# Performance work log

Hardware: AMD Instinct MI355X
Metric: run time of the kernel (lower is better)

Reference implementation:

```python
import jax, jax.numpy as jnp
import numpy as np

N_QUBITS = 4


def _apply_rx(state, theta, wire):
    # state: [B, 2,2,2,2] complex64, theta: [B] real angles; RX on `wire`.
    st = jnp.moveaxis(state, wire + 1, -1)
    bshape = (theta.shape[0],) + (1,) * (st.ndim - 2)
    c = jnp.cos(theta * 0.5).reshape(bshape).astype(jnp.complex64)
    s = (-1j) * jnp.sin(theta * 0.5).reshape(bshape).astype(jnp.complex64)
    new = jnp.stack([c * st[..., 0] + s * st[..., 1],
                     s * st[..., 0] + c * st[..., 1]], axis=-1)
    return jnp.moveaxis(new, -1, wire + 1)


def _apply_cnot(state, control, target):
    st = jnp.moveaxis(state, (control + 1, target + 1), (-2, -1))
    new = jnp.stack([st[..., 0, :], st[..., 1, ::-1]], axis=-2)
    return jnp.moveaxis(new, (-2, -1), (control + 1, target + 1))


def _quantum_gate(angles, thetas):
    # angles: [B, n] data-encoding RX angles; thetas: [n] trainable RX angles.
    B, n = angles.shape
    state = jnp.zeros((B,) + (2,) * n, jnp.complex64)
    state = state.at[(slice(None),) + (0,) * n].set(1.0)  # |0...0>
    for w in range(n):
        state = _apply_rx(state, angles[:, w], w)
    for w in range(n):
        state = _apply_rx(state, jnp.broadcast_to(thetas[w], (B,)), w)
    for w in range(n):
        state = _apply_cnot(state, w, (w + 1) % n)
    probs = jnp.abs(state.reshape(B, 2 ** n)) ** 2  # [B, 16]
    bits = (np.arange(2 ** n)[:, None] >> np.arange(n - 1, -1, -1)[None, :]) & 1
    signs = jnp.asarray(1.0 - 2.0 * bits, jnp.float32)  # [16, n] PauliZ eigvals
    return probs @ signs  # [B, n] <Z_w> expectations


def setup_inputs() -> dict:
    key = jax.random.key(0)
    ks = jax.random.split(key, 12)
    B, D, H, n = 131072, 256, 4, N_QUBITS
    fan_in = D + H
    sc = 1.0 / np.sqrt(fan_in)
    inp = {
        'x': jax.random.normal(ks[0], (B, D), jnp.float32),
        'hx': jax.random.normal(ks[1], (B, H), jnp.float32),
        'cx': jax.random.normal(ks[2], (B, H), jnp.float32),
        'W_f': jax.random.normal(ks[3], (n, fan_in), jnp.float32) * sc,
        'b_f': jnp.zeros((n,), jnp.float32),
        'W_i': jax.random.normal(ks[4], (n, fan_in), jnp.float32) * sc,
        'b_i': jnp.zeros((n,), jnp.float32),
        'W_u': jax.random.normal(ks[5], (n, fan_in), jnp.float32) * sc,
        'b_u': jnp.zeros((n,), jnp.float32),
        'W_o': jax.random.normal(ks[6], (n, fan_in), jnp.float32) * sc,
        'b_o': jnp.zeros((n,), jnp.float32),
        'th_f': jax.random.normal(ks[7], (n,), jnp.float32),
        'th_i': jax.random.normal(ks[8], (n,), jnp.float32),
        'th_u': jax.random.normal(ks[9], (n,), jnp.float32),
        'th_o': jax.random.normal(ks[10], (n,), jnp.float32),
    }
    return inp


def reference(x, hx, cx, W_f, b_f, W_i, b_i, W_u, b_u, W_o, b_o,
              th_f, th_i, th_u, th_o):
    comb = jnp.concatenate([x, hx], axis=1)  # [B, D+H]
    f = jax.nn.sigmoid(_quantum_gate(comb @ W_f.T + b_f, th_f))
    i = jax.nn.sigmoid(_quantum_gate(comb @ W_i.T + b_i, th_i))
    g = jnp.tanh(_quantum_gate(comb @ W_u.T + b_u, th_u))
    o = jax.nn.sigmoid(_quantum_gate(comb @ W_o.T + b_o, th_o))
    c_new = f * cx + i * g
    h_new = o * jnp.tanh(c_new)
    return (h_new, c_new)
```

## Files before the change

kernel.cpp:

```cpp
#include <hip/hip_runtime.h>

#define NB   131072
#define TPB  256
#define FANIN 260

__device__ __forceinline__ float sigm_(float x) { return 1.0f / (1.0f + __expf(-x)); }
__device__ __forceinline__ float tanh_(float x) { return 1.0f - 2.0f / (__expf(2.0f * x) + 1.0f); }

__global__ void qlstm_prep(const float* __restrict__ Wf, const float* __restrict__ bf,
                           const float* __restrict__ Wi, const float* __restrict__ bi,
                           const float* __restrict__ Wu, const float* __restrict__ bu,
                           const float* __restrict__ Wo, const float* __restrict__ bo,
                           const float* __restrict__ thf, const float* __restrict__ thi,
                           const float* __restrict__ thu, const float* __restrict__ tho,
                           float* __restrict__ Wp, float* __restrict__ bth) {
    int t = blockIdx.x * blockDim.x + threadIdx.x;
    if (t < FANIN * 16) {
        int k = t >> 4, gw = t & 15, g = gw >> 2, w = gw & 3;
        const float* Wg = (g == 0) ? Wf : (g == 1) ? Wi : (g == 2) ? Wu : Wo;
        Wp[t] = Wg[w * FANIN + k];
    }
    if (t < 16) {
        int g = t >> 2, w = t & 3;
        const float* bg = (g == 0) ? bf  : (g == 1) ? bi  : (g == 2) ? bu  : bo;
        const float* tg = (g == 0) ? thf : (g == 1) ? thi : (g == 2) ? thu : tho;
        bth[t] = bg[w] + tg[w];
    }
}

__global__ __launch_bounds__(TPB) void qlstm_main(
        const float* __restrict__ x, const float* __restrict__ hx,
        const float* __restrict__ cx, const float* __restrict__ Wp,
        const float* __restrict__ bth, float* __restrict__ out) {
    __shared__ float xs[TPB * 33];

    const int tid  = threadIdx.x;
    const int row0 = blockIdx.x * TPB;
    const int row  = row0 + tid;

    float acc[16];
#pragma unroll
    for (int j = 0; j < 16; ++j) acc[j] = 0.0f;

    const float4* x4 = (const float4*)x;

    for (int stage = 0; stage < 8; ++stage) {
#pragma unroll
        for (int u = 0; u < 8; ++u) {
            int f  = tid + (u << 8);
            int r  = f >> 3;
            int c4 = f & 7;
            float4 v = x4[(size_t)(row0 + r) * 64 + stage * 8 + c4];
            float* dst = &xs[r * 33 + (c4 << 2)];
            dst[0] = v.x; dst[1] = v.y; dst[2] = v.z; dst[3] = v.w;
        }
        __syncthreads();

        const float* xrow = &xs[tid * 33];
        const float* wbase = Wp + stage * 32 * 16;
#pragma unroll
        for (int kk = 0; kk < 32; ++kk) {
            float xv = xrow[kk];
            const float* wp = wbase + kk * 16;
#pragma unroll
            for (int j = 0; j < 16; ++j) acc[j] = fmaf(xv, wp[j], acc[j]);
        }
        __syncthreads();
    }

    float4 hv = ((const float4*)hx)[row];
    {
        const float* wp = Wp + 256 * 16;
#pragma unroll
        for (int j = 0; j < 16; ++j) acc[j] = fmaf(hv.x, wp[j],      acc[j]);
#pragma unroll
        for (int j = 0; j < 16; ++j) acc[j] = fmaf(hv.y, wp[16 + j], acc[j]);
#pragma unroll
        for (int j = 0; j < 16; ++j) acc[j] = fmaf(hv.z, wp[32 + j], acc[j]);
#pragma unroll
        for (int j = 0; j < 16; ++j) acc[j] = fmaf(hv.w, wp[48 + j], acc[j]);
    }

    float co[16];
#pragma unroll
    for (int j = 0; j < 16; ++j) co[j] = __cosf(acc[j] + bth[j]);

    float G[16];
#pragma unroll
    for (int g = 0; g < 4; ++g) {
        float c0 = co[g * 4 + 0], c1 = co[g * 4 + 1];
        float c2 = co[g * 4 + 2], c3 = co[g * 4 + 3];
        float e1 = c0 * c1;
        float e2 = e1 * c2;
        float e3 = e2 * c3;
        float e0 = c1 * c2 * c3;
        G[g * 4 + 0] = e0; G[g * 4 + 1] = e1; G[g * 4 + 2] = e2; G[g * 4 + 3] = e3;
    }

    float4 cxv = ((const float4*)cx)[row];
    float cxa[4] = {cxv.x, cxv.y, cxv.z, cxv.w};

    float hn[4], cn[4];
#pragma unroll
    for (int w = 0; w < 4; ++w) {
        float fg = sigm_(G[0 * 4 + w]);
        float ig = sigm_(G[1 * 4 + w]);
        float ug = tanh_(G[2 * 4 + w]);
        float og = sigm_(G[3 * 4 + w]);
        float c_ = fg * cxa[w] + ig * ug;
        cn[w] = c_;
        hn[w] = og * tanh_(c_);
    }

    ((float4*)out)[row]      = make_float4(hn[0], hn[1], hn[2], hn[3]);
    ((float4*)out)[NB + row] = make_float4(cn[0], cn[1], cn[2], cn[3]);
}

extern "C" void kernel_launch(void* const* d_in, const int* in_sizes, int n_in,
                              void* d_out, int out_size, void* d_ws, size_t ws_size,
                              hipStream_t stream) {
    const float* x   = (const float*)d_in[0];
    const float* hx  = (const float*)d_in[1];
    const float* cx  = (const float*)d_in[2];
    const float* Wf  = (const float*)d_in[3];
    const float* bf  = (const float*)d_in[4];
    const float* Wi  = (const float*)d_in[5];
    const float* bi  = (const float*)d_in[6];
    const float* Wu  = (const float*)d_in[7];
    const float* bu  = (const float*)d_in[8];
    const float* Wo  = (const float*)d_in[9];
    const float* bo  = (const float*)d_in[10];
    const float* thf = (const float*)d_in[11];
    const float* thi = (const float*)d_in[12];
    const float* thu = (const float*)d_in[13];
    const float* tho = (const float*)d_in[14];

    float* Wp  = (float*)d_ws;
    float* bth = Wp + FANIN * 16;

    qlstm_prep<<<(FANIN * 16 + TPB - 1) / TPB, TPB, 0, stream>>>(
        Wf, bf, Wi, bi, Wu, bu, Wo, bo, thf, thi, thu, tho, Wp, bth);

    qlstm_main<<<NB / TPB, TPB, 0, stream>>>(
        x, hx, cx, Wp, bth, (float*)d_out);
}
```

Measured before the change: 223.9 us.

## Fuse weight prep into main kernel and double-buffer x loads via registers

Removes the separate prep kernel: each block transposes the gate weights and bias+theta into shared memory itself, so the launch and the global-memory weight reads are dropped. x tiles are prefetched into registers for the next stage while the current stage computes from shared memory, and shared loads become float4 with a padded stride. The cost is more shared memory per block (about 53KB), redundant weight transposition in every block, and more registers held for the prefetch, which may reduce occupancy.

```diff
diff --git a/kernel.cpp b/kernel.cpp
--- a/kernel.cpp
+++ b/kernel.cpp
@@ -1,84 +1,122 @@
 #include <hip/hip_runtime.h>
 
-#define NB   131072
-#define TPB  256
+#define NB    131072
+#define TPB   256
 #define FANIN 260
+#define PADF4 9
 
 __device__ __forceinline__ float sigm_(float x) { return 1.0f / (1.0f + __expf(-x)); }
 __device__ __forceinline__ float tanh_(float x) { return 1.0f - 2.0f / (__expf(2.0f * x) + 1.0f); }
 
-__global__ void qlstm_prep(const float* __restrict__ Wf, const float* __restrict__ bf,
-                           const float* __restrict__ Wi, const float* __restrict__ bi,
-                           const float* __restrict__ Wu, const float* __restrict__ bu,
-                           const float* __restrict__ Wo, const float* __restrict__ bo,
-                           const float* __restrict__ thf, const float* __restrict__ thi,
-                           const float* __restrict__ thu, const float* __restrict__ tho,
-                           float* __restrict__ Wp, float* __restrict__ bth) {
-    int t = blockIdx.x * blockDim.x + threadIdx.x;
-    if (t < FANIN * 16) {
-        int k = t >> 4, gw = t & 15, g = gw >> 2, w = gw & 3;
-        const float* Wg = (g == 0) ? Wf : (g == 1) ? Wi : (g == 2) ? Wu : Wo;
-        Wp[t] = Wg[w * FANIN + k];
-    }
-    if (t < 16) {
-        int g = t >> 2, w = t & 3;
-        const float* bg = (g == 0) ? bf  : (g == 1) ? bi  : (g == 2) ? bu  : bo;
-        const float* tg = (g == 0) ? thf : (g == 1) ? thi : (g == 2) ? thu : tho;
-        bth[t] = bg[w] + tg[w];
-    }
-}
-
-__global__ __launch_bounds__(TPB) void qlstm_main(
-        const float* __restrict__ x, const float* __restrict__ hx,
-        const float* __restrict__ cx, const float* __restrict__ Wp,
-        const float* __restrict__ bth, float* __restrict__ out) {
-    __shared__ float xs[TPB * 33];
+__global__ __launch_bounds__(TPB, 2) void qlstm_fused(
+        const float* __restrict__ x,  const float* __restrict__ hx,
+        const float* __restrict__ cx,
+        const float* __restrict__ Wf, const float* __restrict__ bf,
+        const float* __restrict__ Wi, const float* __restrict__ bi,
+        const float* __restrict__ Wu, const float* __restrict__ bu,
+        const float* __restrict__ Wo, const float* __restrict__ bo,
+        const float* __restrict__ thf, const float* __restrict__ thi,
+        const float* __restrict__ thu, const float* __restrict__ tho,
+        float* __restrict__ out) {
+    __shared__ float xs[TPB * 36];
+    __shared__ float wl[FANIN * 16];
+    __shared__ float bth[16];
 
     const int tid  = threadIdx.x;
     const int row0 = blockIdx.x * TPB;
     const int row  = row0 + tid;
 
+    const float4* x4  = (const float4*)x;
+    float4*       xs4 = (float4*)xs;
+
+    float4 hv  = ((const float4*)hx)[row];
+    float4 cxv = ((const float4*)cx)[row];
+
+    float4 pf[8];
+#pragma unroll
+    for (int u = 0; u < 8; ++u) {
+        int f = tid + (u << 8);
+        pf[u] = x4[(size_t)(row0 + (f >> 3)) * 64 + (f & 7)];
+    }
+
+    for (int k = tid; k < FANIN; k += TPB) {
+#pragma unroll
+        for (int g = 0; g < 4; ++g) {
+            const float* Wg = (g == 0) ? Wf : (g == 1) ? Wi : (g == 2) ? Wu : Wo;
+#pragma unroll
+            for (int w = 0; w < 4; ++w)
+                wl[k * 16 + g * 4 + w] = Wg[w * FANIN + k];
+        }
+    }
+    if (tid < 16) {
+        int g = tid >> 2, w = tid & 3;
+        const float* bg = (g == 0) ? bf  : (g == 1) ? bi  : (g == 2) ? bu  : bo;
+        const float* tg = (g == 0) ? thf : (g == 1) ? thi : (g == 2) ? thu : tho;
+        bth[tid] = bg[w] + tg[w];
+    }
+
+#pragma unroll
+    for (int u = 0; u < 8; ++u) {
+        int f = tid + (u << 8);
+        xs4[(f >> 3) * PADF4 + (f & 7)] = pf[u];
+    }
+    __syncthreads();
+
     float acc[16];
 #pragma unroll
     for (int j = 0; j < 16; ++j) acc[j] = 0.0f;
 
-    const float4* x4 = (const float4*)x;
+    const float4* wl4 = (const float4*)wl;
 
+#pragma unroll
     for (int stage = 0; stage < 8; ++stage) {
+        if (stage < 7) {
 #pragma unroll
-        for (int u = 0; u < 8; ++u) {
-            int f  = tid + (u << 8);
-            int r  = f >> 3;
-            int c4 = f & 7;
-            float4 v = x4[(size_t)(row0 + r) * 64 + stage * 8 + c4];
-            float* dst = &xs[r * 33 + (c4 << 2)];
-            dst[0] = v.x; dst[1] = v.y; dst[2] = v.z; dst[3] = v.w;
+            for (int u = 0; u < 8; ++u) {
+                int f = tid + (u << 8);
+                pf[u] = x4[(size_t)(row0 + (f >> 3)) * 64 + (stage + 1) * 8 + (f & 7)];
+            }
+        }
+#pragma unroll
+        for (int kk4 = 0; kk4 < 8; ++kk4) {
+            float4 xv = xs4[tid * PADF4 + kk4];
+#pragma unroll
+            for (int m = 0; m < 4; ++m) {
+                float xe = (m == 0) ? xv.x : (m == 1) ? xv.y : (m == 2) ? xv.z : xv.w;
+                int k = stage * 32 + kk4 * 4 + m;
+#pragma unroll
+                for (int j4 = 0; j4 < 4; ++j4) {
+                    float4 w = wl4[k * 4 + j4];
+                    acc[j4 * 4 + 0] = fmaf(xe, w.x, acc[j4 * 4 + 0]);
+                    acc[j4 * 4 + 1] = fmaf(xe, w.y, acc[j4 * 4 + 1]);
+                    acc[j4 * 4 + 2] = fmaf(xe, w.z, acc[j4 * 4 + 2]);
+                    acc[j4 * 4 + 3] = fmaf(xe, w.w, acc[j4 * 4 + 3]);
+                }
+            }
         }
         __syncthreads();
-
-        const float* xrow = &xs[tid * 33];
-        const float* wbase = Wp + stage * 32 * 16;
+        if (stage < 7) {
 #pragma unroll
-        for (int kk = 0; kk < 32; ++kk) {
-            float xv = xrow[kk];
-            const float* wp = wbase + kk * 16;
-#pragma unroll
-            for (int j = 0; j < 16; ++j) acc[j] = fmaf(xv, wp[j], acc[j]);
+            for (int u = 0; u < 8; ++u) {
+                int f = tid + (u << 8);
+                xs4[(f >> 3) * PADF4 + (f & 7)] = pf[u];
+            }
+            __syncthreads();
         }
-        __syncthreads();
     }
 
-    float4 hv = ((const float4*)hx)[row];
-    {
-        const float* wp = Wp + 256 * 16;
 #pragma unroll
-        for (int j = 0; j < 16; ++j) acc[j] = fmaf(hv.x, wp[j],      acc[j]);
+    for (int m = 0; m < 4; ++m) {
+        float he = (m == 0) ? hv.x : (m == 1) ? hv.y : (m == 2) ? hv.z : hv.w;
+        int k = 256 + m;
 #pragma unroll
-        for (int j = 0; j < 16; ++j) acc[j] = fmaf(hv.y, wp[16 + j], acc[j]);
-#pragma unroll
-        for (int j = 0; j < 16; ++j) acc[j] = fmaf(hv.z, wp[32 + j], acc[j]);
-#pragma unroll
-        for (int j = 0; j < 16; ++j) acc[j] = fmaf(hv.w, wp[48 + j], acc[j]);
+        for (int j4 = 0; j4 < 4; ++j4) {
+            float4 w = wl4[k * 4 + j4];
+            acc[j4 * 4 + 0] = fmaf(he, w.x, acc[j4 * 4 + 0]);
+            acc[j4 * 4 + 1] = fmaf(he, w.y, acc[j4 * 4 + 1]);
+            acc[j4 * 4 + 2] = fmaf(he, w.z, acc[j4 * 4 + 2]);
+            acc[j4 * 4 + 3] = fmaf(he, w.w, acc[j4 * 4 + 3]);
+        }
     }
 
     float co[16];
@@ -97,9 +135,7 @@
         G[g * 4 + 0] = e0; G[g * 4 + 1] = e1; G[g * 4 + 2] = e2; G[g * 4 + 3] = e3;
     }
 
-    float4 cxv = ((const float4*)cx)[row];
     float cxa[4] = {cxv.x, cxv.y, cxv.z, cxv.w};
-
     float hn[4], cn[4];
 #pragma unroll
     for (int w = 0; w < 4; ++w) {
@@ -135,12 +171,9 @@
     const float* thu = (const float*)d_in[13];
     const float* tho = (const float*)d_in[14];
 
-    float* Wp  = (float*)d_ws;
-    float* bth = Wp + FANIN * 16;
+    (void)d_ws; (void)ws_size;
 
-    qlstm_prep<<<(FANIN * 16 + TPB - 1) / TPB, TPB, 0, stream>>>(
-        Wf, bf, Wi, bi, Wu, bu, Wo, bo, thf, thi, thu, tho, Wp, bth);
-
-    qlstm_main<<<NB / TPB, TPB, 0, stream>>>(
-        x, hx, cx, Wp, bth, (float*)d_out);
+    qlstm_fused<<<NB / TPB, TPB, 0, stream>>>(
+        x, hx, cx, Wf, bf, Wi, bi, Wu, bu, Wo, bo,
+        thf, thi, thu, tho, (float*)d_out);
 }
```

New measurement: 330.8 us. 1.48x slower.

## Use single-wavefront blocks with register-prefetched double-buffered LDS staging

Applied to the files above, without the earlier changes.

Shrinks blocks to 64 threads, one wavefront, and drops the __syncthreads barriers. The next x tile is prefetched into registers while the current tile is consumed from a second LDS buffer. LDS is repacked as float4 rows with a 9-float4 stride so each thread reads its row with wide loads, and the hx/cx loads are hoisted to the start. The aim is to overlap global load latency with the FMA work and cut barrier and LDS instruction overhead. It relies on wavefront-synchronous behaviour with no explicit barrier, and it raises register pressure from the prefetch registers.

```diff
diff --git a/kernel.cpp b/kernel.cpp
--- a/kernel.cpp
+++ b/kernel.cpp
@@ -1,8 +1,9 @@
 #include <hip/hip_runtime.h>
 
-#define NB   131072
-#define TPB  256
+#define NB    131072
+#define TPB   64
 #define FANIN 260
+#define SROWF4 9
 
 __device__ __forceinline__ float sigm_(float x) { return 1.0f / (1.0f + __expf(-x)); }
 __device__ __forceinline__ float tanh_(float x) { return 1.0f - 2.0f / (__expf(2.0f * x) + 1.0f); }
@@ -32,43 +33,72 @@
         const float* __restrict__ x, const float* __restrict__ hx,
         const float* __restrict__ cx, const float* __restrict__ Wp,
         const float* __restrict__ bth, float* __restrict__ out) {
-    __shared__ float xs[TPB * 33];
+    __shared__ float4 xs4[2 * TPB * SROWF4];
 
-    const int tid  = threadIdx.x;
+    const int lane = threadIdx.x;
     const int row0 = blockIdx.x * TPB;
-    const int row  = row0 + tid;
+    const int row  = row0 + lane;
+
+    const float4* x4 = (const float4*)x;
+
+    float4 hv  = ((const float4*)hx)[row];
+    float4 cxv = ((const float4*)cx)[row];
+
+    float4 pf[8];
+#pragma unroll
+    for (int u = 0; u < 8; ++u) {
+        int f = lane + (u << 6);
+        pf[u] = x4[(size_t)(row0 + (f >> 3)) * 64 + (f & 7)];
+    }
+#pragma unroll
+    for (int u = 0; u < 8; ++u) {
+        int f = lane + (u << 6);
+        xs4[(f >> 3) * SROWF4 + (f & 7)] = pf[u];
+    }
 
     float acc[16];
 #pragma unroll
     for (int j = 0; j < 16; ++j) acc[j] = 0.0f;
 
-    const float4* x4 = (const float4*)x;
+#pragma unroll 2
+    for (int stage = 0; stage < 8; ++stage) {
+        float4* cur = &xs4[(stage & 1)        * (TPB * SROWF4)];
+        float4* nxt = &xs4[((stage + 1) & 1)  * (TPB * SROWF4)];
 
-    for (int stage = 0; stage < 8; ++stage) {
+        if (stage < 7) {
 #pragma unroll
-        for (int u = 0; u < 8; ++u) {
-            int f  = tid + (u << 8);
-            int r  = f >> 3;
-            int c4 = f & 7;
-            float4 v = x4[(size_t)(row0 + r) * 64 + stage * 8 + c4];
-            float* dst = &xs[r * 33 + (c4 << 2)];
-            dst[0] = v.x; dst[1] = v.y; dst[2] = v.z; dst[3] = v.w;
+            for (int u = 0; u < 8; ++u) {
+                int f = lane + (u << 6);
+                pf[u] = x4[(size_t)(row0 + (f >> 3)) * 64 + (stage + 1) * 8 + (f & 7)];
+            }
         }
-        __syncthreads();
 
-        const float* xrow = &xs[tid * 33];
+        float4 xr[8];
+#pragma unroll
+        for (int k4 = 0; k4 < 8; ++k4) xr[k4] = cur[lane * SROWF4 + k4];
+
         const float* wbase = Wp + stage * 32 * 16;
 #pragma unroll
-        for (int kk = 0; kk < 32; ++kk) {
-            float xv = xrow[kk];
-            const float* wp = wbase + kk * 16;
+        for (int k4 = 0; k4 < 8; ++k4) {
 #pragma unroll
-            for (int j = 0; j < 16; ++j) acc[j] = fmaf(xv, wp[j], acc[j]);
+            for (int m = 0; m < 4; ++m) {
+                float xe = (m == 0) ? xr[k4].x : (m == 1) ? xr[k4].y
+                         : (m == 2) ? xr[k4].z : xr[k4].w;
+                const float* wp = wbase + (k4 * 4 + m) * 16;
+#pragma unroll
+                for (int j = 0; j < 16; ++j) acc[j] = fmaf(xe, wp[j], acc[j]);
+            }
         }
-        __syncthreads();
+
+        if (stage < 7) {
+#pragma unroll
+            for (int u = 0; u < 8; ++u) {
+                int f = lane + (u << 6);
+                nxt[(f >> 3) * SROWF4 + (f & 7)] = pf[u];
+            }
+        }
     }
 
-    float4 hv = ((const float4*)hx)[row];
     {
         const float* wp = Wp + 256 * 16;
 #pragma unroll
@@ -97,9 +127,7 @@
         G[g * 4 + 0] = e0; G[g * 4 + 1] = e1; G[g * 4 + 2] = e2; G[g * 4 + 3] = e3;
     }
 
-    float4 cxv = ((const float4*)cx)[row];
     float cxa[4] = {cxv.x, cxv.y, cxv.z, cxv.w};
-
     float hn[4], cn[4];
 #pragma unroll
     for (int w = 0; w < 4; ++w) {
@@ -138,7 +166,7 @@
     float* Wp  = (float*)d_ws;
     float* bth = Wp + FANIN * 16;
 
-    qlstm_prep<<<(FANIN * 16 + TPB - 1) / TPB, TPB, 0, stream>>>(
+    qlstm_prep<<<(FANIN * 16 + 255) / 256, 256, 0, stream>>>(
         Wf, bf, Wi, bi, Wu, bu, Wo, bo, thf, thi, thu, tho, Wp, bth);
 
     qlstm_main<<<NB / TPB, TPB, 0, stream>>>(
```

Result: slower. 274.8 us (+22.8%).

## Split K across two waves with direct register loads and LDS reduction

Applied to the files above, without the earlier changes.

Each 128-thread block now handles 64 rows. Each wave takes half of the 256 input features, reading x straight into registers with float4 loads double-buffered across four chunks, so the shared-memory transpose stage and its barriers are gone. Wave 1 adds the hx term and writes its partial sums to LDS, and wave 0 reduces them and does the gate epilogue. Per-thread global reads become strided by row (1 KB apart), which may hurt coalescing, and half the threads sit idle during the epilogue.

```diff
diff --git a/kernel.cpp b/kernel.cpp
--- a/kernel.cpp
+++ b/kernel.cpp
@@ -1,7 +1,7 @@
 #include <hip/hip_runtime.h>
 
-#define NB   131072
-#define TPB  256
+#define NB    131072
+#define TPB   128
 #define FANIN 260
 
 __device__ __forceinline__ float sigm_(float x) { return 1.0f / (1.0f + __expf(-x)); }
@@ -28,48 +28,62 @@
     }
 }
 
-__global__ __launch_bounds__(TPB) void qlstm_main(
+__device__ __forceinline__ void consume8(const float4 (&b)[8],
+                                         const float* __restrict__ wb,
+                                         float (&acc)[16]) {
+#pragma unroll
+    for (int u = 0; u < 8; ++u) {
+#pragma unroll
+        for (int m = 0; m < 4; ++m) {
+            float xe = (m == 0) ? b[u].x : (m == 1) ? b[u].y
+                     : (m == 2) ? b[u].z : b[u].w;
+            const float* wp = wb + (u * 4 + m) * 16;
+#pragma unroll
+            for (int j = 0; j < 16; ++j) acc[j] = fmaf(xe, wp[j], acc[j]);
+        }
+    }
+}
+
+__global__ __launch_bounds__(TPB, 4) void qlstm_main(
         const float* __restrict__ x, const float* __restrict__ hx,
         const float* __restrict__ cx, const float* __restrict__ Wp,
         const float* __restrict__ bth, float* __restrict__ out) {
-    __shared__ float xs[TPB * 33];
+    __shared__ float accx[64 * 16];
 
     const int tid  = threadIdx.x;
-    const int row0 = blockIdx.x * TPB;
-    const int row  = row0 + tid;
+    const int lane = tid & 63;
+    const int wv   = tid >> 6;
+    const int wvu  = __builtin_amdgcn_readfirstlane(wv);
+    const int row0 = blockIdx.x * 64;
+    const int row  = row0 + lane;
+
+    const float4* xr = (const float4*)x + (size_t)row * 64 + wvu * 32;
+    const float*  wW = Wp + wvu * (4 * 512);
+
+    float4 hv = make_float4(0.f, 0.f, 0.f, 0.f);
+    float4 cxv = make_float4(0.f, 0.f, 0.f, 0.f);
+    if (wvu == 1) hv  = ((const float4*)hx)[row];
+    else          cxv = ((const float4*)cx)[row];
 
     float acc[16];
 #pragma unroll
     for (int j = 0; j < 16; ++j) acc[j] = 0.0f;
 
-    const float4* x4 = (const float4*)x;
+    float4 A[8], B[8];
+#pragma unroll
+    for (int u = 0; u < 8; ++u) A[u] = xr[u];
+#pragma unroll
+    for (int u = 0; u < 8; ++u) B[u] = xr[8 + u];
+    consume8(A, wW + 0 * 512, acc);
+#pragma unroll
+    for (int u = 0; u < 8; ++u) A[u] = xr[16 + u];
+    consume8(B, wW + 1 * 512, acc);
+#pragma unroll
+    for (int u = 0; u < 8; ++u) B[u] = xr[24 + u];
+    consume8(A, wW + 2 * 512, acc);
+    consume8(B, wW + 3 * 512, acc);
 
-    for (int stage = 0; stage < 8; ++stage) {
-#pragma unroll
-        for (int u = 0; u < 8; ++u) {
-            int f  = tid + (u << 8);
-            int r  = f >> 3;
-            int c4 = f & 7;
-            float4 v = x4[(size_t)(row0 + r) * 64 + stage * 8 + c4];
-            float* dst = &xs[r * 33 + (c4 << 2)];
-            dst[0] = v.x; dst[1] = v.y; dst[2] = v.z; dst[3] = v.w;
-        }
-        __syncthreads();
-
-        const float* xrow = &xs[tid * 33];
-        const float* wbase = Wp + stage * 32 * 16;
-#pragma unroll
-        for (int kk = 0; kk < 32; ++kk) {
-            float xv = xrow[kk];
-            const float* wp = wbase + kk * 16;
-#pragma unroll
-            for (int j = 0; j < 16; ++j) acc[j] = fmaf(xv, wp[j], acc[j]);
-        }
-        __syncthreads();
-    }
-
-    float4 hv = ((const float4*)hx)[row];
-    {
+    if (wvu == 1) {
         const float* wp = Wp + 256 * 16;
 #pragma unroll
         for (int j = 0; j < 16; ++j) acc[j] = fmaf(hv.x, wp[j],      acc[j]);
@@ -79,41 +93,55 @@
         for (int j = 0; j < 16; ++j) acc[j] = fmaf(hv.z, wp[32 + j], acc[j]);
 #pragma unroll
         for (int j = 0; j < 16; ++j) acc[j] = fmaf(hv.w, wp[48 + j], acc[j]);
+#pragma unroll
+        for (int j4 = 0; j4 < 4; ++j4)
+            ((float4*)accx)[lane * 4 + j4] =
+                make_float4(acc[j4 * 4 + 0], acc[j4 * 4 + 1],
+                            acc[j4 * 4 + 2], acc[j4 * 4 + 3]);
     }
+    __syncthreads();
+    if (wvu == 0) {
+#pragma unroll
+        for (int j4 = 0; j4 < 4; ++j4) {
+            float4 p = ((const float4*)accx)[lane * 4 + j4];
+            acc[j4 * 4 + 0] += p.x;
+            acc[j4 * 4 + 1] += p.y;
+            acc[j4 * 4 + 2] += p.z;
+            acc[j4 * 4 + 3] += p.w;
+        }
 
-    float co[16];
+        float co[16];
 #pragma unroll
-    for (int j = 0; j < 16; ++j) co[j] = __cosf(acc[j] + bth[j]);
+        for (int j = 0; j < 16; ++j) co[j] = __cosf(acc[j] + bth[j]);
 
-    float G[16];
+        float G[16];
 #pragma unroll
-    for (int g = 0; g < 4; ++g) {
-        float c0 = co[g * 4 + 0], c1 = co[g * 4 + 1];
-        float c2 = co[g * 4 + 2], c3 = co[g * 4 + 3];
-        float e1 = c0 * c1;
-        float e2 = e1 * c2;
-        float e3 = e2 * c3;
-        float e0 = c1 * c2 * c3;
-        G[g * 4 + 0] = e0; G[g * 4 + 1] = e1; G[g * 4 + 2] = e2; G[g * 4 + 3] = e3;
+        for (int g = 0; g < 4; ++g) {
+            float c0 = co[g * 4 + 0], c1 = co[g * 4 + 1];
+            float c2 = co[g * 4 + 2], c3 = co[g * 4 + 3];
+            float e1 = c0 * c1;
+            float e2 = e1 * c2;
+            float e3 = e2 * c3;
+            float e0 = c1 * c2 * c3;
+            G[g * 4 + 0] = e0; G[g * 4 + 1] = e1; G[g * 4 + 2] = e2; G[g * 4 + 3] = e3;
+        }
+
+        float cxa[4] = {cxv.x, cxv.y, cxv.z, cxv.w};
+        float hn[4], cn[4];
+#pragma unroll
+        for (int w = 0; w < 4; ++w) {
+            float fg = sigm_(G[0 * 4 + w]);
+            float ig = sigm_(G[1 * 4 + w]);
+            float ug = tanh_(G[2 * 4 + w]);
+            float og = sigm_(G[3 * 4 + w]);
+            float c_ = fg * cxa[w] + ig * ug;
+            cn[w] = c_;
+            hn[w] = og * tanh_(c_);
+        }
+
+        ((float4*)out)[row]      = make_float4(hn[0], hn[1], hn[2], hn[3]);
+        ((float4*)out)[NB + row] = make_float4(cn[0], cn[1], cn[2], cn[3]);
     }
-
-    float4 cxv = ((const float4*)cx)[row];
-    float cxa[4] = {cxv.x, cxv.y, cxv.z, cxv.w};
-
-    float hn[4], cn[4];
-#pragma unroll
-    for (int w = 0; w < 4; ++w) {
-        float fg = sigm_(G[0 * 4 + w]);
-        float ig = sigm_(G[1 * 4 + w]);
-        float ug = tanh_(G[2 * 4 + w]);
-        float og = sigm_(G[3 * 4 + w]);
-        float c_ = fg * cxa[w] + ig * ug;
-        cn[w] = c_;
-        hn[w] = og * tanh_(c_);
-    }
-
-    ((float4*)out)[row]      = make_float4(hn[0], hn[1], hn[2], hn[3]);
-    ((float4*)out)[NB + row] = make_float4(cn[0], cn[1], cn[2], cn[3]);
 }
 
 extern "C" void kernel_launch(void* const* d_in, const int* in_sizes, int n_in,
@@ -138,9 +166,9 @@
     float* Wp  = (float*)d_ws;
     float* bth = Wp + FANIN * 16;
 
-    qlstm_prep<<<(FANIN * 16 + TPB - 1) / TPB, TPB, 0, stream>>>(
+    qlstm_prep<<<(FANIN * 16 + 255) / 256, 256, 0, stream>>>(
         Wf, bf, Wi, bi, Wu, bu, Wo, bo, thf, thi, thu, tho, Wp, bth);
 
-    qlstm_main<<<NB / TPB, TPB, 0, stream>>>(
+    qlstm_main<<<NB / 64, TPB, 0, stream>>>(
         x, hx, cx, Wp, bth, (float*)d_out);
 }
```

After: 228.2 us. About the same (+2.0%).
